# Performance work log

Measured on AMD Instinct MI355X. Metric: run time of the kernel, lower is better.

## Reference

```python
import jax, jax.numpy as jnp
import numpy as np

B, S, D = 8, 4096, 1024
N_LEVELS = 8
L = 8
EPS = 1e-3        # FSQ eps (bound shrink)
LN_EPS = 1e-5     # torch LayerNorm default eps


def setup_inputs() -> dict:
    key = jax.random.key(0)
    k1, k2 = jax.random.split(key)
    regrs = jax.random.normal(k1, (B, S, D), dtype=jnp.float32)
    ln_w = jnp.ones((D,), dtype=jnp.float32)
    ln_b = jnp.zeros((D,), dtype=jnp.float32)
    # nn.Linear(d_model, n_levels, bias=False): weight shape [n_levels, d_model]
    W = jax.random.normal(k2, (N_LEVELS, D), dtype=jnp.float32) * (1.0 / np.sqrt(D))
    return {"regrs": regrs, "ln_w": ln_w, "ln_b": ln_b, "W": W}


def reference(regrs, ln_w, ln_b, W):
    # LayerNorm over last dim (biased variance, matching torch)
    mean = jnp.mean(regrs, axis=-1, keepdims=True)
    var = jnp.mean(jnp.square(regrs - mean), axis=-1, keepdims=True)
    x = (regrs - mean) * jax.lax.rsqrt(var + LN_EPS) * ln_w + ln_b
    # skinny projection to n_levels channels
    z = jnp.einsum('bsd,nd->bsn', x, W)  # [B,S,N_LEVELS]
    half_l = L * (1.0 - EPS) / 2.0
    bounded = half_l * jnp.tanh(z)
    # round with straight-through estimator
    code = bounded + jax.lax.stop_gradient(jnp.round(bounded) - bounded)
    return code
```

## Files before the change

kernel.cpp:

```cpp
#include <hip/hip_runtime.h>
#include <math.h>

#define NLEV 8
#define D_DIM 1024

struct TB  { float  t[8]; };
struct TBD { double t[8]; };

typedef __attribute__((ext_vector_type(8))) short bf16x8;
typedef __attribute__((ext_vector_type(4))) float f32x4;

__device__ __forceinline__ unsigned bf16_rne_bits(float f) {
    const unsigned u = __float_as_uint(f);
    return (u + 0x7FFFu + ((u >> 16) & 1u)) >> 16;
}
__device__ __forceinline__ float bf16_bits_to_f(unsigned h) {
    return __uint_as_float(h << 16);
}

template<int CTRL>
__device__ __forceinline__ float ror_add(float v) {
    int r = __builtin_amdgcn_update_dpp(0, __float_as_int(v), CTRL, 0xF, 0xF, true);
    return v + __int_as_float(r);
}
__device__ __forceinline__ float red16(float v) {
    v = ror_add<0x121>(v); v = ror_add<0x122>(v);
    v = ror_add<0x124>(v); v = ror_add<0x128>(v);
    return v;
}
__device__ __forceinline__ float wave_allreduce(float v) {
    v = red16(v);
    v += __shfl_xor(v, 16, 64);
    v += __shfl_xor(v, 32, 64);
    return v;
}

__device__ __forceinline__ void repair_row_reload(
        int row, const float* __restrict__ xg,
        const float* __restrict__ gg, const float* __restrict__ bg,
        const float* __restrict__ Wg, float* __restrict__ outg,
        const TBD& tbd, int lane)
{
    const float4* xb4 = (const float4*)(xg + (size_t)row * D_DIM);
    const float4 x0 = xb4[lane];
    const float4 x1 = xb4[64 + lane];
    const float4 x2 = xb4[128 + lane];
    const float4 x3 = xb4[192 + lane];

    double ds = 0.0, dsq = 0.0;
    #pragma unroll
    for (int j = 0; j < 4; ++j) {
        const float4 a = (j == 0) ? x0 : (j == 1) ? x1 : (j == 2) ? x2 : x3;
        const double v0 = (double)a.x, v1 = (double)a.y;
        const double v2 = (double)a.z, v3 = (double)a.w;
        ds += ((v0 + v1) + (v2 + v3));
        dsq = fma(v0, v0, dsq); dsq = fma(v1, v1, dsq);
        dsq = fma(v2, v2, dsq); dsq = fma(v3, v3, dsq);
    }
    #pragma unroll
    for (int off = 32; off >= 1; off >>= 1) {
        ds  += __shfl_xor(ds, off, 64);
        dsq += __shfl_xor(dsq, off, 64);
    }
    const double mean = ds * (1.0 / 1024.0);
    const double var  = dsq * (1.0 / 1024.0) - mean * mean;
    const double rstd = 1.0 / sqrt(var + 1e-5);

    double dacc[NLEV];
    #pragma unroll
    for (int n = 0; n < NLEV; ++n) dacc[n] = 0.0;
    #pragma unroll
    for (int j = 0; j < 4; ++j) {
        const int col = j * 256 + lane * 4;
        const float4 a = (j == 0) ? x0 : (j == 1) ? x1 : (j == 2) ? x2 : x3;
        const float4 g4 = *(const float4*)(gg + col);
        const float4 b4 = *(const float4*)(bg + col);
        const double y0 = fma(((double)a.x - mean) * rstd, (double)g4.x, (double)b4.x);
        const double y1 = fma(((double)a.y - mean) * rstd, (double)g4.y, (double)b4.y);
        const double y2 = fma(((double)a.z - mean) * rstd, (double)g4.z, (double)b4.z);
        const double y3 = fma(((double)a.w - mean) * rstd, (double)g4.w, (double)b4.w);
        #pragma unroll
        for (int n = 0; n < NLEV; ++n) {
            const float4 w4 = *(const float4*)(Wg + n * D_DIM + col);
            dacc[n] = fma(y0, (double)w4.x, dacc[n]);
            dacc[n] = fma(y1, (double)w4.y, dacc[n]);
            dacc[n] = fma(y2, (double)w4.z, dacc[n]);
            dacc[n] = fma(y3, (double)w4.w, dacc[n]);
        }
    }
    #pragma unroll
    for (int off = 32; off >= 1; off >>= 1) {
        #pragma unroll
        for (int n = 0; n < NLEV; ++n) dacc[n] += __shfl_xor(dacc[n], off, 64);
    }
    if (lane < NLEV) {
        double a0d = (lane & 4) ? dacc[4] : dacc[0];
        double a1d = (lane & 4) ? dacc[5] : dacc[1];
        double a2d = (lane & 4) ? dacc[6] : dacc[2];
        double a3d = (lane & 4) ? dacc[7] : dacc[3];
        double b0d = (lane & 2) ? a2d : a0d;
        double b1d = (lane & 2) ? a3d : a1d;
        const double z = (lane & 1) ? b1d : b0d;
        int c = 0;
        #pragma unroll
        for (int k = 0; k < 8; ++k) c += (z > tbd.t[k]) ? 1 : 0;
        outg[(size_t)row * NLEV + lane] = (float)(c - 4);
    }
}

__global__ __launch_bounds__(256) void fsq_mfma(
        const float* __restrict__ xg,
        const float* __restrict__ gg,
        const float* __restrict__ bg,
        const float* __restrict__ Wg,
        float* __restrict__ outg,
        int nrows, TB tb, TBD tbd)
{
    __shared__ __align__(16) short Bf[32 * 64 * 8];
    __shared__ float redc1[4][NLEV];
    __shared__ float redc0[4][NLEV];

    const int tid  = (int)threadIdx.x;
    const int lane = tid & 63;
    const int wv   = tid >> 6;

    {
        const int col = tid * 4;
        const float4 g4 = *(const float4*)(gg + col);
        const float4 b4 = *(const float4*)(bg + col);
        float pc1[NLEV], pc0[NLEV];
        #pragma unroll
        for (int n = 0; n < NLEV; ++n) {
            const float4 w4 = *(const float4*)(Wg + n * D_DIM + col);
            pc1[n] = (g4.x * w4.x + g4.y * w4.y) + (g4.z * w4.z + g4.w * w4.w);
            pc0[n] = (b4.x * w4.x + b4.y * w4.y) + (b4.z * w4.z + b4.w * w4.w);
        }
        #pragma unroll
        for (int n = 0; n < NLEV; ++n) {
            pc1[n] = wave_allreduce(pc1[n]);
            pc0[n] = wave_allreduce(pc0[n]);
        }
        if (lane == 0) {
            #pragma unroll
            for (int n = 0; n < NLEV; ++n) { redc1[wv][n] = pc1[n]; redc0[wv][n] = pc0[n]; }
        }
    }

    #pragma unroll 1
    for (int i = 0; i < 8; ++i) {
        const int slot = tid + i * 256;
        const int ks   = slot >> 6;
        const int ln   = slot & 63;
        const int cn   = ln & 15;
        const int n    = cn & 7;
        const int k0   = ks * 32 + (ln >> 4) * 8;
        const float4 ga  = *(const float4*)(gg + k0);
        const float4 gb2 = *(const float4*)(gg + k0 + 4);
        const float4 wa  = *(const float4*)(Wg + n * D_DIM + k0);
        const float4 wb  = *(const float4*)(Wg + n * D_DIM + k0 + 4);
        float v[8] = { ga.x * wa.x,  ga.y * wa.y,  ga.z * wa.z,  ga.w * wa.w,
                       gb2.x * wb.x, gb2.y * wb.y, gb2.z * wb.z, gb2.w * wb.w };
        bf16x8 frag;
        if (cn < 8) {
            #pragma unroll
            for (int e = 0; e < 8; ++e) frag[e] = (short)bf16_rne_bits(v[e]);
        } else {
            #pragma unroll
            for (int e = 0; e < 8; ++e) {
                const unsigned hb = bf16_rne_bits(v[e]);
                frag[e] = (short)bf16_rne_bits(v[e] - bf16_bits_to_f(hb));
            }
        }
        *(bf16x8*)&Bf[slot * 8] = frag;
    }
    __syncthreads();

    const int nsel = lane & 7;
    const float C1sel = redc1[0][nsel] + redc1[1][nsel] + redc1[2][nsel] + redc1[3][nsel];
    const float C0sel = redc0[0][nsel] + redc0[1][nsel] + redc0[2][nsel] + redc0[3][nsel];

    const int row0  = (int)blockIdx.x * 64 + wv * 16;
    const int myrow = row0 + (lane & 15);
    const int rowc  = (myrow < nrows) ? myrow : (nrows - 1);
    const float* xrow = xg + (size_t)rowc * D_DIM + (lane >> 4) * 8;

    f32x4 acc1 = {0.f, 0.f, 0.f, 0.f};
    f32x4 acc2 = {0.f, 0.f, 0.f, 0.f};
    float s = 0.f, sq = 0.f;

    for (int ks = 0; ks < 32; ++ks) {
        const float4 xa  = *(const float4*)(xrow + ks * 32);
        const float4 xb2 = *(const float4*)(xrow + ks * 32 + 4);
        s += ((xa.x + xa.y) + (xa.z + xa.w)) + ((xb2.x + xb2.y) + (xb2.z + xb2.w));
        sq = fmaf(xa.x, xa.x, sq);   sq = fmaf(xa.y, xa.y, sq);
        sq = fmaf(xa.z, xa.z, sq);   sq = fmaf(xa.w, xa.w, sq);
        sq = fmaf(xb2.x, xb2.x, sq); sq = fmaf(xb2.y, xb2.y, sq);
        sq = fmaf(xb2.z, xb2.z, sq); sq = fmaf(xb2.w, xb2.w, sq);

        const float xs0[8] = { xa.x, xa.y, xa.z, xa.w, xb2.x, xb2.y, xb2.z, xb2.w };
        bf16x8 xh, xl;
        #pragma unroll
        for (int e = 0; e < 8; ++e) {
            const unsigned hb = bf16_rne_bits(xs0[e]);
            xh[e] = (short)hb;
            xl[e] = (short)bf16_rne_bits(xs0[e] - bf16_bits_to_f(hb));
        }
        const bf16x8 bfr = *(const bf16x8*)&Bf[(ks * 64 + lane) * 8];
        acc1 = __builtin_amdgcn_mfma_f32_16x16x32_bf16(xh, bfr, acc1, 0, 0, 0);
        acc2 = __builtin_amdgcn_mfma_f32_16x16x32_bf16(xl, bfr, acc2, 0, 0, 0);
    }

    s  += __shfl_xor(s, 16, 64);  s  += __shfl_xor(s, 32, 64);
    sq += __shfl_xor(sq, 16, 64); sq += __shfl_xor(sq, 32, 64);
    const float mean_me = s * (1.0f / 1024.0f);
    const float var_me  = sq * (1.0f / 1024.0f) - mean_me * mean_me;
    const float rstd_me = 1.0f / sqrtf(var_me + 1e-5f);

    unsigned rmaskw = 0u;
    const int grp = lane >> 4;
    #pragma unroll
    for (int r = 0; r < 4; ++r) {
        const float t = acc1[r] + acc2[r];
        const float S = t + __shfl_xor(t, 8, 64);
        const int srcl = (grp << 2) | r;
        const float mean_r = __shfl(mean_me, srcl, 64);
        const float rstd_r = __shfl(rstd_me, srcl, 64);
        const float z = rstd_r * (S - mean_r * C1sel) + C0sel;

        int cnt = 0; float mind = 1e30f;
        #pragma unroll
        for (int k = 0; k < 8; ++k) {
            cnt += (z > tb.t[k]) ? 1 : 0;
            mind = fminf(mind, fabsf(z - tb.t[k]));
        }
        const int orow = row0 + grp * 4 + r;
        const bool rok = (orow < nrows);
        if (((lane & 15) < 8) && rok)
            outg[(size_t)orow * NLEV + (lane & 7)] = (float)(cnt - 4);
        const bool fl = ((lane & 15) < 8) && rok && (mind < 1.0e-3f);
        const unsigned long long bal = __ballot(fl);
        #pragma unroll
        for (int g2 = 0; g2 < 4; ++g2)
            if ((bal >> (g2 * 16)) & 0xFFFFull) rmaskw |= 1u << (g2 * 4 + r);
    }

    while (rmaskw) {
        const int p = __builtin_ctz(rmaskw);
        rmaskw &= rmaskw - 1u;
        repair_row_reload(row0 + p, xg, gg, bg, Wg, outg, tbd, lane);
    }
}

extern "C" void kernel_launch(void* const* d_in, const int* in_sizes, int n_in,
                              void* d_out, int out_size, void* d_ws, size_t ws_size,
                              hipStream_t stream) {
    (void)n_in; (void)out_size; (void)d_ws; (void)ws_size;
    const float* regrs = (const float*)d_in[0];
    const float* ln_w  = (const float*)d_in[1];
    const float* ln_b  = (const float*)d_in[2];
    const float* W     = (const float*)d_in[3];
    float* out = (float*)d_out;

    const int nrows = in_sizes[0] / D_DIM;
    const int nblocks = (nrows + 63) / 64;

    TB tb; TBD tbd;
    for (int k = 0; k < 8; ++k) {
        const double y = ((double)k - 3.5) / 3.996;
        tbd.t[k] = atanh(y);
        tb.t[k]  = (float)tbd.t[k];
    }

    fsq_mfma<<<nblocks, 256, 0, stream>>>(regrs, ln_w, ln_b, W, out, nrows, tb, tbd);
}
```

Baseline: 236.5 us.

## Split each row tile's K dimension across two waves with LDS reduction

Each block now covers 32 rows instead of 64. Two waves share a 16-row tile, and each handles half of the 1024-wide reduction. Partial MFMA sums and the per-row sum and sum-of-squares go through shared memory, and one wave finishes the LayerNorm, thresholding and repair. This doubles the block count and shortens the serial K loop per wave, adding latency hiding and memory-level parallelism. The cost is that every block repeats the W/gamma/beta preprocessing over half as many rows, and there is an extra barrier plus LDS traffic.

Measured after the change: 302.2 us. 1.28x slower.

```diff
diff --git a/kernel.cpp b/kernel.cpp
--- a/kernel.cpp
+++ b/kernel.cpp
@@ -108,7 +108,7 @@
     }
 }
 
-__global__ __launch_bounds__(256) void fsq_mfma(
+__global__ __launch_bounds__(256, 4) void fsq_mfma(
         const float* __restrict__ xg,
         const float* __restrict__ gg,
         const float* __restrict__ bg,
@@ -119,10 +119,14 @@
     __shared__ __align__(16) short Bf[32 * 64 * 8];
     __shared__ float redc1[4][NLEV];
     __shared__ float redc0[4][NLEV];
+    __shared__ float Sbuf[2][2][16][NLEV];
+    __shared__ float msbuf[2][2][16][2];
 
     const int tid  = (int)threadIdx.x;
     const int lane = tid & 63;
     const int wv   = tid >> 6;
+    const int t    = wv >> 1;
+    const int h    = wv & 1;
 
     {
         const int col = tid * 4;
@@ -179,16 +183,17 @@
     const float C1sel = redc1[0][nsel] + redc1[1][nsel] + redc1[2][nsel] + redc1[3][nsel];
     const float C0sel = redc0[0][nsel] + redc0[1][nsel] + redc0[2][nsel] + redc0[3][nsel];
 
-    const int row0  = (int)blockIdx.x * 64 + wv * 16;
+    const int row0  = (int)blockIdx.x * 32 + t * 16;
     const int myrow = row0 + (lane & 15);
     const int rowc  = (myrow < nrows) ? myrow : (nrows - 1);
-    const float* xrow = xg + (size_t)rowc * D_DIM + (lane >> 4) * 8;
+    const float* xrow = xg + (size_t)rowc * D_DIM + (lane >> 4) * 8 + h * 512;
 
     f32x4 acc1 = {0.f, 0.f, 0.f, 0.f};
     f32x4 acc2 = {0.f, 0.f, 0.f, 0.f};
     float s = 0.f, sq = 0.f;
 
-    for (int ks = 0; ks < 32; ++ks) {
+    #pragma unroll 2
+    for (int ks = 0; ks < 16; ++ks) {
         const float4 xa  = *(const float4*)(xrow + ks * 32);
         const float4 xb2 = *(const float4*)(xrow + ks * 32 + 4);
         s += ((xa.x + xa.y) + (xa.z + xa.w)) + ((xb2.x + xb2.y) + (xb2.z + xb2.w));
@@ -205,49 +210,61 @@
             xh[e] = (short)hb;
             xl[e] = (short)bf16_rne_bits(xs0[e] - bf16_bits_to_f(hb));
         }
-        const bf16x8 bfr = *(const bf16x8*)&Bf[(ks * 64 + lane) * 8];
+        const bf16x8 bfr = *(const bf16x8*)&Bf[((h * 16 + ks) * 64 + lane) * 8];
         acc1 = __builtin_amdgcn_mfma_f32_16x16x32_bf16(xh, bfr, acc1, 0, 0, 0);
         acc2 = __builtin_amdgcn_mfma_f32_16x16x32_bf16(xl, bfr, acc2, 0, 0, 0);
     }
 
     s  += __shfl_xor(s, 16, 64);  s  += __shfl_xor(s, 32, 64);
     sq += __shfl_xor(sq, 16, 64); sq += __shfl_xor(sq, 32, 64);
-    const float mean_me = s * (1.0f / 1024.0f);
-    const float var_me  = sq * (1.0f / 1024.0f) - mean_me * mean_me;
-    const float rstd_me = 1.0f / sqrtf(var_me + 1e-5f);
-
-    unsigned rmaskw = 0u;
+    if (lane < 16) { msbuf[t][h][lane][0] = s; msbuf[t][h][lane][1] = sq; }
+
     const int grp = lane >> 4;
     #pragma unroll
     for (int r = 0; r < 4; ++r) {
-        const float t = acc1[r] + acc2[r];
-        const float S = t + __shfl_xor(t, 8, 64);
-        const int srcl = (grp << 2) | r;
-        const float mean_r = __shfl(mean_me, srcl, 64);
-        const float rstd_r = __shfl(rstd_me, srcl, 64);
-        const float z = rstd_r * (S - mean_r * C1sel) + C0sel;
-
-        int cnt = 0; float mind = 1e30f;
-        #pragma unroll
-        for (int k = 0; k < 8; ++k) {
-            cnt += (z > tb.t[k]) ? 1 : 0;
-            mind = fminf(mind, fabsf(z - tb.t[k]));
-        }
-        const int orow = row0 + grp * 4 + r;
-        const bool rok = (orow < nrows);
-        if (((lane & 15) < 8) && rok)
-            outg[(size_t)orow * NLEV + (lane & 7)] = (float)(cnt - 4);
-        const bool fl = ((lane & 15) < 8) && rok && (mind < 1.0e-3f);
-        const unsigned long long bal = __ballot(fl);
-        #pragma unroll
-        for (int g2 = 0; g2 < 4; ++g2)
-            if ((bal >> (g2 * 16)) & 0xFFFFull) rmaskw |= 1u << (g2 * 4 + r);
-    }
-
-    while (rmaskw) {
-        const int p = __builtin_ctz(rmaskw);
-        rmaskw &= rmaskw - 1u;
-        repair_row_reload(row0 + p, xg, gg, bg, Wg, outg, tbd, lane);
+        const float tt = acc1[r] + acc2[r];
+        const float S = tt + __shfl_xor(tt, 8, 64);
+        if ((lane & 15) < 8) Sbuf[t][h][grp * 4 + r][lane & 7] = S;
+    }
+    __syncthreads();
+
+    if (h == 0) {
+        const int r0a = lane >> 3;
+        const int n   = lane & 7;
+        unsigned rmaskw = 0u;
+
+        #pragma unroll
+        for (int half = 0; half < 2; ++half) {
+            const int row = r0a + half * 8;
+            const float S   = Sbuf[t][0][row][n] + Sbuf[t][1][row][n];
+            const float sT  = msbuf[t][0][row][0] + msbuf[t][1][row][0];
+            const float sqT = msbuf[t][0][row][1] + msbuf[t][1][row][1];
+            const float mean = sT * (1.0f / 1024.0f);
+            const float var  = sqT * (1.0f / 1024.0f) - mean * mean;
+            const float rstd = 1.0f / sqrtf(var + 1e-5f);
+            const float z = rstd * (S - mean * C1sel) + C0sel;
+
+            int cnt = 0; float mind = 1e30f;
+            #pragma unroll
+            for (int k = 0; k < 8; ++k) {
+                cnt += (z > tb.t[k]) ? 1 : 0;
+                mind = fminf(mind, fabsf(z - tb.t[k]));
+            }
+            const int orow = row0 + row;
+            const bool rok = (orow < nrows);
+            if (rok) outg[(size_t)orow * NLEV + n] = (float)(cnt - 4);
+            const bool fl = rok && (mind < 1.0e-3f);
+            const unsigned long long bal = __ballot(fl);
+            #pragma unroll
+            for (int r = 0; r < 8; ++r)
+                if ((bal >> (r * 8)) & 0xFFull) rmaskw |= 1u << (half * 8 + r);
+        }
+
+        while (rmaskw) {
+            const int p = __builtin_ctz(rmaskw);
+            rmaskw &= rmaskw - 1u;
+            repair_row_reload(row0 + p, xg, gg, bg, Wg, outg, tbd, lane);
+        }
     }
 }
 
@@ -262,7 +279,7 @@
     float* out = (float*)d_out;
 
     const int nrows = in_sizes[0] / D_DIM;
-    const int nblocks = (nrows + 63) / 64;
+    const int nblocks = (nrows + 31) / 32;
 
     TB tb; TBD tbd;
     for (int k = 0; k < 8; ++k) {
```
